# Performance work log

Hardware: AMD Instinct MI355X
Metric: run time of the kernel (lower is better)

Reference implementation:

```python
import jax, jax.numpy as jnp
import numpy as np

WS = 7        # window_size
NH = 3        # num_heads


def setup_inputs() -> dict:
    key = jax.random.key(0)
    ks = jax.random.split(key, 5)
    B, H, W, C = 8, 224, 224, 96
    s = 1.0 / np.sqrt(C)
    x = jax.random.normal(ks[0], (B, H, W, C), dtype=jnp.float32)
    qkv_w = jax.random.normal(ks[1], (C, 3 * C), dtype=jnp.float32) * s
    qkv_b = jnp.zeros((3 * C,), dtype=jnp.float32)
    proj_w = jax.random.normal(ks[2], (C, C), dtype=jnp.float32) * s
    proj_b = jnp.zeros((C,), dtype=jnp.float32)
    return {"x": x, "qkv_w": qkv_w, "qkv_b": qkv_b, "proj_w": proj_w, "proj_b": proj_b}


def reference(x, qkv_w, qkv_b, proj_w, proj_b):
    B, H, W, C = x.shape
    ws, nh = WS, NH
    hd = C // nh
    pad_h = (ws - H % ws) % ws
    pad_w = (ws - W % ws) % ws
    x = jnp.pad(x, ((0, 0), (0, pad_h), (0, pad_w), (0, 0)))
    Hp, Wp = x.shape[1], x.shape[2]
    # window partition: [B,Hp,Wp,C] -> [B*nWh*nWw, ws*ws, C]
    xw = x.reshape(B, Hp // ws, ws, Wp // ws, ws, C)
    xw = xw.transpose(0, 1, 3, 2, 4, 5).reshape(-1, ws * ws, C)
    nW = xw.shape[0]
    qkv = xw @ qkv_w + qkv_b                      # [nW, ws*ws, 3C]
    q, k, v = jnp.split(qkv, 3, axis=-1)
    def heads(t):
        return t.reshape(nW, ws * ws, nh, hd).transpose(0, 2, 1, 3)  # [nW,nh,L,hd]
    q, k, v = heads(q), heads(k), heads(v)
    scale = 1.0 / np.sqrt(hd).astype(np.float32)
    attn = jnp.einsum('whld,whmd->whlm', q, k) * scale
    attn = jax.nn.softmax(attn, axis=-1)
    o = jnp.einsum('whlm,whmd->whld', attn, v)    # [nW,nh,L,hd]
    o = o.transpose(0, 2, 1, 3).reshape(nW, ws * ws, C)
    o = o @ proj_w + proj_b
    # window merge: inverse of partition
    o = o.reshape(B, Hp // ws, Wp // ws, ws, ws, C)
    o = o.transpose(0, 1, 3, 2, 4, 5).reshape(B, Hp, Wp, C)
    return o[:, :H, :W, :]
```

## Files before the change

kernel.cpp:

```cpp
#include <hip/hip_runtime.h>
#include <stdint.h>

typedef __bf16 bf16;
typedef __bf16 bf16x4 __attribute__((ext_vector_type(4)));
typedef __bf16 bf16x8 __attribute__((ext_vector_type(8)));
typedef float  f32x4  __attribute__((ext_vector_type(4)));

#define MFMA16(a,b,c) __builtin_amdgcn_mfma_f32_16x16x32_bf16((a),(b),(c),0,0,0)

#define XS_STR 104
#define QK_STR 200
#define SB_STR 72
#define S_HEAD 4608

__global__ void prep_weights(const float* __restrict__ qkv_w,
                             const float* __restrict__ proj_w,
                             bf16* __restrict__ wT) {
    int i = blockIdx.x * 256 + threadIdx.x;
    if (i < 288 * 96) {
        int j = i / 96, c = i - j * 96;
        wT[i] = (bf16)qkv_w[c * 288 + j];
    } else if (i < 288 * 96 + 96 * 96) {
        int t = i - 288 * 96;
        int j = t / 96, c = t - j * 96;
        wT[i] = (bf16)proj_w[c * 96 + j];
    }
}

__global__ __launch_bounds__(256, 4)
void win_attn_kernel(const float* __restrict__ x,
                     const float* __restrict__ qkv_b,
                     const float* __restrict__ proj_b,
                     const bf16* __restrict__ qkvwT,
                     const bf16* __restrict__ projwT,
                     float* __restrict__ out)
{
    __shared__ bf16 ldsA[64 * XS_STR];
    __shared__ bf16 ldsB[3 * 64 * SB_STR];

    const int tid  = threadIdx.x;
    const int wid  = tid >> 6;
    const int lane = tid & 63;
    const int lm   = lane & 15;
    const int lq   = lane >> 4;

    const int wi = blockIdx.x;
    const int b  = wi >> 10;
    const int wr = wi & 1023;
    const int h0 = (wr >> 5) * 7;
    const int w0 = (wr & 31) * 7;

    {
        const float* xbase = x + ((size_t)(b * 224 + h0) * 224 + w0) * 96;
        #pragma unroll
        for (int kk = 0; kk < 3; ++kk) {
            const int t   = tid + kk * 256;
            const int pix = t / 12;
            const int f8  = t - pix * 12;
            bf16x8 bv = {};
            if (pix < 49) {
                const int pr = pix / 7, pc = pix - pr * 7;
                const float* p = xbase + ((size_t)pr * 224 + pc) * 96 + f8 * 8;
                const float4 v0 = *(const float4*)p;
                const float4 v1 = *(const float4*)(p + 4);
                bv = (bf16x8){ (bf16)v0.x, (bf16)v0.y, (bf16)v0.z, (bf16)v0.w,
                               (bf16)v1.x, (bf16)v1.y, (bf16)v1.z, (bf16)v1.w };
            }
            *(bf16x8*)&ldsA[pix * XS_STR + f8 * 8] = bv;
        }
    }
    __syncthreads();

    bf16x8 afr[4][3];
    #pragma unroll
    for (int tt = 0; tt < 4; ++tt)
        #pragma unroll
        for (int ks = 0; ks < 3; ++ks)
            afr[tt][ks] = *(const bf16x8*)&ldsA[(tt * 16 + lm) * XS_STR + ks * 32 + lq * 8];
    __syncthreads();

    {
        const float Cs = 0.2550348607051632f;
        for (int ft = wid; ft < 18; ft += 4) {
            bf16x8 wf[3];
            #pragma unroll
            for (int ks = 0; ks < 3; ++ks)
                wf[ks] = *(const bf16x8*)&qkvwT[(size_t)(ft * 16 + lm) * 96 + ks * 32 + lq * 8];
            if (ft < 12) {
                const f32x4 bias4 = *(const f32x4*)(qkv_b + ft * 16 + lq * 4);
                f32x4 acc[4];
                #pragma unroll
                for (int tt = 0; tt < 4; ++tt) acc[tt] = bias4;
                #pragma unroll
                for (int ks = 0; ks < 3; ++ks)
                    #pragma unroll
                    for (int tt = 0; tt < 4; ++tt)
                        acc[tt] = MFMA16(wf[ks], afr[tt][ks], acc[tt]);
                const bool isq = (ft < 6);
                #pragma unroll
                for (int tt = 0; tt < 4; ++tt) {
                    f32x4 a = acc[tt];
                    if (isq) a *= Cs;
                    bf16x4 pv = { (bf16)a[0], (bf16)a[1], (bf16)a[2], (bf16)a[3] };
                    *(bf16x4*)&ldsB[(tt * 16 + lm) * QK_STR + ft * 16 + lq * 4] = pv;
                }
            } else {
                const int d0 = (ft - 12) * 16 + lm;
                const float bias = qkv_b[192 + d0];
                f32x4 acc[4];
                #pragma unroll
                for (int mt = 0; mt < 4; ++mt) acc[mt] = (f32x4){bias, bias, bias, bias};
                #pragma unroll
                for (int ks = 0; ks < 3; ++ks)
                    #pragma unroll
                    for (int mt = 0; mt < 4; ++mt)
                        acc[mt] = MFMA16(afr[mt][ks], wf[ks], acc[mt]);
                #pragma unroll
                for (int mt = 0; mt < 4; ++mt) {
                    bf16x4 pv = { (bf16)acc[mt][0], (bf16)acc[mt][1],
                                  (bf16)acc[mt][2], (bf16)acc[mt][3] };
                    const int grp = mt * 2 + (lq >> 1);
                    *(bf16x4*)&ldsA[d0 * 64 + ((grp ^ (d0 & 7)) << 3) + ((lq & 1) << 2)] = pv;
                }
            }
        }
    }
    __syncthreads();

    bf16x8 aq[4], bk[4];
    if (wid < 3) {
        const int h = wid;
        #pragma unroll
        for (int qt = 0; qt < 4; ++qt)
            aq[qt] = *(const bf16x8*)&ldsB[(qt * 16 + lm) * QK_STR + h * 32 + lq * 8];
        #pragma unroll
        for (int kt = 0; kt < 4; ++kt)
            bk[kt] = *(const bf16x8*)&ldsB[(kt * 16 + lm) * QK_STR + 96 + h * 32 + lq * 8];
    }
    __syncthreads();

    f32x4 oacc[2][4];
    f32x4 rin;
    if (wid < 3) {
        const int h = wid;
        const f32x4 zf = {0.f, 0.f, 0.f, 0.f};
        bf16* Sb = &ldsB[h * S_HEAD];
        f32x4 sums = zf;

        #pragma unroll
        for (int kt = 0; kt < 4; ++kt) {
            f32x4 s[4];
            #pragma unroll
            for (int qt = 0; qt < 4; ++qt)
                s[qt] = MFMA16(bk[kt], aq[qt], zf);
            if (kt < 3) {
                #pragma unroll
                for (int qt = 0; qt < 4; ++qt) {
                    const float p0 = exp2f(s[qt][0]);
                    const float p1 = exp2f(s[qt][1]);
                    const float p2 = exp2f(s[qt][2]);
                    const float p3 = exp2f(s[qt][3]);
                    sums[qt] += (p0 + p1) + (p2 + p3);
                    bf16x4 pv = { (bf16)p0, (bf16)p1, (bf16)p2, (bf16)p3 };
                    *(bf16x4*)&Sb[(qt * 16 + lm) * SB_STR + kt * 16 + lq * 4] = pv;
                }
            } else {
                #pragma unroll
                for (int qt = 0; qt < 4; ++qt) {
                    const float p0 = (lq == 0) ? exp2f(s[qt][0]) : 0.f;
                    sums[qt] += p0;
                    bf16x4 pv = { (bf16)p0, (bf16)0.f, (bf16)0.f, (bf16)0.f };
                    *(bf16x4*)&Sb[(qt * 16 + lm) * SB_STR + 48 + lq * 4] = pv;
                }
            }
        }
        #pragma unroll
        for (int qt = 0; qt < 4; ++qt) {
            float sm = sums[qt];
            sm += __shfl_xor(sm, 16);
            sm += __shfl_xor(sm, 32);
            rin[qt] = __builtin_amdgcn_rcpf(sm);
        }
        asm volatile("s_waitcnt lgkmcnt(0)" ::: "memory");

        #pragma unroll
        for (int f2 = 0; f2 < 2; ++f2)
            #pragma unroll
            for (int qt = 0; qt < 4; ++qt) oacc[f2][qt] = zf;
        #pragma unroll
        for (int ks = 0; ks < 2; ++ks) {
            bf16x8 av[2], ap[4];
            #pragma unroll
            for (int f2 = 0; f2 < 2; ++f2) {
                const int frow = h * 32 + f2 * 16 + lm;
                av[f2] = *(const bf16x8*)&ldsA[frow * 64 + (((ks * 4 + lq) ^ (frow & 7)) << 3)];
            }
            #pragma unroll
            for (int qt = 0; qt < 4; ++qt)
                ap[qt] = *(const bf16x8*)&Sb[(qt * 16 + lm) * SB_STR + ks * 32 + lq * 8];
            #pragma unroll
            for (int f2 = 0; f2 < 2; ++f2)
                #pragma unroll
                for (int qt = 0; qt < 4; ++qt)
                    oacc[f2][qt] = MFMA16(av[f2], ap[qt], oacc[f2][qt]);
        }
        #pragma unroll
        for (int f2 = 0; f2 < 2; ++f2)
            #pragma unroll
            for (int qt = 0; qt < 4; ++qt)
                oacc[f2][qt] *= rin[qt];
    }
    __syncthreads();

    if (wid < 3) {
        const int h = wid;
        #pragma unroll
        for (int f2 = 0; f2 < 2; ++f2)
            #pragma unroll
            for (int qt = 0; qt < 4; ++qt) {
                const f32x4 a = oacc[f2][qt];
                bf16x4 ov = { (bf16)a[0], (bf16)a[1], (bf16)a[2], (bf16)a[3] };
                *(bf16x4*)&ldsB[(qt * 16 + lm) * XS_STR + h * 32 + f2 * 16 + lq * 4] = ov;
            }
    }
    __syncthreads();

    {
        const int tt = wid;
        bf16x8 of[3];
        #pragma unroll
        for (int ks = 0; ks < 3; ++ks)
            of[ks] = *(const bf16x8*)&ldsB[(tt * 16 + lm) * XS_STR + ks * 32 + lq * 8];
        const int token = tt * 16 + lm;
        const int tv = (token < 49) ? token : 0;
        const int pr = tv / 7, pc = tv - pr * 7;
        float* obase = out + ((size_t)(b * 224 + h0 + pr) * 224 + (w0 + pc)) * 96 + lq * 4;
        #pragma unroll
        for (int ft = 0; ft < 6; ++ft) {
            bf16x8 wp[3];
            #pragma unroll
            for (int ks = 0; ks < 3; ++ks)
                wp[ks] = *(const bf16x8*)&projwT[(size_t)(ft * 16 + lm) * 96 + ks * 32 + lq * 8];
            f32x4 acc = *(const f32x4*)(proj_b + ft * 16 + lq * 4);
            #pragma unroll
            for (int ks = 0; ks < 3; ++ks)
                acc = MFMA16(wp[ks], of[ks], acc);
            if (token < 49)
                *(f32x4*)(obase + ft * 16) = acc;
        }
    }
}

extern "C" void kernel_launch(void* const* d_in, const int* in_sizes, int n_in,
                              void* d_out, int out_size, void* d_ws, size_t ws_size,
                              hipStream_t stream) {
    const float* x      = (const float*)d_in[0];
    const float* qkv_w  = (const float*)d_in[1];
    const float* qkv_b  = (const float*)d_in[2];
    const float* proj_w = (const float*)d_in[3];
    const float* proj_b = (const float*)d_in[4];
    float* out = (float*)d_out;

    bf16* wT = (bf16*)d_ws;
    const int n_w = 288 * 96 + 96 * 96;
    prep_weights<<<(n_w + 255) / 256, 256, 0, stream>>>(qkv_w, proj_w, wT);
    win_attn_kernel<<<8192, 256, 0, stream>>>(x, qkv_b, proj_b,
                                              wT, wT + 288 * 96, out);
}
```

Before: 334.5 us.

## Split attention by query tiles across all four waves and shrink LDS footprint

Reassigns the attention stage so each of the four waves handles one 16-row query tile across all three heads, instead of three waves each handling one head over all query tiles. Softmax probabilities now stay in registers and are fed straight into the PV MFMA, which removes the score round-trip through LDS and two barriers. LDS is consolidated into one 49-row-padded buffer (~32KB) and launch bounds rise to 5 blocks per CU to raise occupancy. The cost is some repeated K/V fragment loads per wave, more register pressure under the tighter bound, and garbage padding rows handled by masking.

```diff
diff --git a/kernel.cpp b/kernel.cpp
--- a/kernel.cpp
+++ b/kernel.cpp
@@ -8,10 +8,11 @@
 
 #define MFMA16(a,b,c) __builtin_amdgcn_mfma_f32_16x16x32_bf16((a),(b),(c),0,0,0)
 
-#define XS_STR 104
-#define QK_STR 200
-#define SB_STR 72
-#define S_HEAD 4608
+#define ST 104
+#define QB 0
+#define KB 5096
+#define VB 10192
+#define LDS_ELEMS 16336
 
 __global__ void prep_weights(const float* __restrict__ qkv_w,
                              const float* __restrict__ proj_w,
@@ -27,7 +28,7 @@
     }
 }
 
-__global__ __launch_bounds__(256, 4)
+__global__ __launch_bounds__(256, 5)
 void win_attn_kernel(const float* __restrict__ x,
                      const float* __restrict__ qkv_b,
                      const float* __restrict__ proj_b,
@@ -35,8 +36,7 @@
                      const bf16* __restrict__ projwT,
                      float* __restrict__ out)
 {
-    __shared__ bf16 ldsA[64 * XS_STR];
-    __shared__ bf16 ldsB[3 * 64 * SB_STR];
+    __shared__ bf16 lds[LDS_ELEMS];
 
     const int tid  = threadIdx.x;
     const int wid  = tid >> 6;
@@ -52,21 +52,15 @@
 
     {
         const float* xbase = x + ((size_t)(b * 224 + h0) * 224 + w0) * 96;
-        #pragma unroll
-        for (int kk = 0; kk < 3; ++kk) {
-            const int t   = tid + kk * 256;
-            const int pix = t / 12;
-            const int f8  = t - pix * 12;
-            bf16x8 bv = {};
-            if (pix < 49) {
-                const int pr = pix / 7, pc = pix - pr * 7;
-                const float* p = xbase + ((size_t)pr * 224 + pc) * 96 + f8 * 8;
-                const float4 v0 = *(const float4*)p;
-                const float4 v1 = *(const float4*)(p + 4);
-                bv = (bf16x8){ (bf16)v0.x, (bf16)v0.y, (bf16)v0.z, (bf16)v0.w,
-                               (bf16)v1.x, (bf16)v1.y, (bf16)v1.z, (bf16)v1.w };
-            }
-            *(bf16x8*)&ldsA[pix * XS_STR + f8 * 8] = bv;
+        for (int t = tid; t < 49 * 12; t += 256) {
+            const int pix = t / 12, f8 = t - pix * 12;
+            const int pr = pix / 7, pc = pix - pr * 7;
+            const float* p = xbase + ((size_t)pr * 224 + pc) * 96 + f8 * 8;
+            const float4 v0 = *(const float4*)p;
+            const float4 v1 = *(const float4*)(p + 4);
+            bf16x8 bv = { (bf16)v0.x, (bf16)v0.y, (bf16)v0.z, (bf16)v0.w,
+                          (bf16)v1.x, (bf16)v1.y, (bf16)v1.z, (bf16)v1.w };
+            *(bf16x8*)&lds[VB + pix * ST + f8 * 8] = bv;
         }
     }
     __syncthreads();
@@ -75,8 +69,12 @@
     #pragma unroll
     for (int tt = 0; tt < 4; ++tt)
         #pragma unroll
-        for (int ks = 0; ks < 3; ++ks)
-            afr[tt][ks] = *(const bf16x8*)&ldsA[(tt * 16 + lm) * XS_STR + ks * 32 + lq * 8];
+        for (int ks = 0; ks < 3; ++ks) {
+            if (tt < 3 || lm == 0)
+                afr[tt][ks] = *(const bf16x8*)&lds[VB + (tt * 16 + lm) * ST + ks * 32 + lq * 8];
+            else
+                afr[tt][ks] = (bf16x8){};
+        }
     __syncthreads();
 
     {
@@ -97,12 +95,16 @@
                     for (int tt = 0; tt < 4; ++tt)
                         acc[tt] = MFMA16(wf[ks], afr[tt][ks], acc[tt]);
                 const bool isq = (ft < 6);
+                const int base = isq ? QB : KB;
+                const int col  = (isq ? ft : ft - 6) * 16 + lq * 4;
                 #pragma unroll
                 for (int tt = 0; tt < 4; ++tt) {
-                    f32x4 a = acc[tt];
-                    if (isq) a *= Cs;
-                    bf16x4 pv = { (bf16)a[0], (bf16)a[1], (bf16)a[2], (bf16)a[3] };
-                    *(bf16x4*)&ldsB[(tt * 16 + lm) * QK_STR + ft * 16 + lq * 4] = pv;
+                    if (tt < 3 || lm == 0) {
+                        f32x4 a = acc[tt];
+                        if (isq) a *= Cs;
+                        bf16x4 pv = { (bf16)a[0], (bf16)a[1], (bf16)a[2], (bf16)a[3] };
+                        *(bf16x4*)&lds[base + (tt * 16 + lm) * ST + col] = pv;
+                    }
                 }
             } else {
                 const int d0 = (ft - 12) * 16 + lm;
@@ -119,109 +121,62 @@
                 for (int mt = 0; mt < 4; ++mt) {
                     bf16x4 pv = { (bf16)acc[mt][0], (bf16)acc[mt][1],
                                   (bf16)acc[mt][2], (bf16)acc[mt][3] };
-                    const int grp = mt * 2 + (lq >> 1);
-                    *(bf16x4*)&ldsA[d0 * 64 + ((grp ^ (d0 & 7)) << 3) + ((lq & 1) << 2)] = pv;
+                    const int g = (mt >> 1) * 4 + lq;
+                    *(bf16x4*)&lds[VB + d0 * 64 + ((g ^ (d0 & 7)) << 3) + ((mt & 1) << 2)] = pv;
                 }
             }
         }
     }
     __syncthreads();
 
-    bf16x8 aq[4], bk[4];
-    if (wid < 3) {
-        const int h = wid;
-        #pragma unroll
-        for (int qt = 0; qt < 4; ++qt)
-            aq[qt] = *(const bf16x8*)&ldsB[(qt * 16 + lm) * QK_STR + h * 32 + lq * 8];
-        #pragma unroll
-        for (int kt = 0; kt < 4; ++kt)
-            bk[kt] = *(const bf16x8*)&ldsB[(kt * 16 + lm) * QK_STR + 96 + h * 32 + lq * 8];
-    }
-    __syncthreads();
-
-    f32x4 oacc[2][4];
-    f32x4 rin;
-    if (wid < 3) {
-        const int h = wid;
+    {
+        const int qrow = wid * 16 + lm;
         const f32x4 zf = {0.f, 0.f, 0.f, 0.f};
-        bf16* Sb = &ldsB[h * S_HEAD];
-        f32x4 sums = zf;
-
-        #pragma unroll
-        for (int kt = 0; kt < 4; ++kt) {
-            f32x4 s[4];
-            #pragma unroll
-            for (int qt = 0; qt < 4; ++qt)
-                s[qt] = MFMA16(bk[kt], aq[qt], zf);
-            if (kt < 3) {
-                #pragma unroll
-                for (int qt = 0; qt < 4; ++qt) {
-                    const float p0 = exp2f(s[qt][0]);
-                    const float p1 = exp2f(s[qt][1]);
-                    const float p2 = exp2f(s[qt][2]);
-                    const float p3 = exp2f(s[qt][3]);
-                    sums[qt] += (p0 + p1) + (p2 + p3);
-                    bf16x4 pv = { (bf16)p0, (bf16)p1, (bf16)p2, (bf16)p3 };
-                    *(bf16x4*)&Sb[(qt * 16 + lm) * SB_STR + kt * 16 + lq * 4] = pv;
-                }
-            } else {
-                #pragma unroll
-                for (int qt = 0; qt < 4; ++qt) {
-                    const float p0 = (lq == 0) ? exp2f(s[qt][0]) : 0.f;
-                    sums[qt] += p0;
-                    bf16x4 pv = { (bf16)p0, (bf16)0.f, (bf16)0.f, (bf16)0.f };
-                    *(bf16x4*)&Sb[(qt * 16 + lm) * SB_STR + 48 + lq * 4] = pv;
-                }
+        #pragma unroll
+        for (int h = 0; h < 3; ++h) {
+            const bf16x8 aqv = *(const bf16x8*)&lds[QB + qrow * ST + h * 32 + lq * 8];
+            bf16x8 bkv[4];
+            #pragma unroll
+            for (int kt = 0; kt < 4; ++kt)
+                bkv[kt] = *(const bf16x8*)&lds[KB + (kt * 16 + lm) * ST + h * 32 + lq * 8];
+            f32x4 s0 = MFMA16(bkv[0], aqv, zf);
+            f32x4 s1 = MFMA16(bkv[1], aqv, zf);
+            f32x4 s2 = MFMA16(bkv[2], aqv, zf);
+            f32x4 s3 = MFMA16(bkv[3], aqv, zf);
+            float p0  = exp2f(s0[0]), p1  = exp2f(s0[1]), p2  = exp2f(s0[2]), p3  = exp2f(s0[3]);
+            float p4  = exp2f(s1[0]), p5  = exp2f(s1[1]), p6  = exp2f(s1[2]), p7  = exp2f(s1[3]);
+            float p8  = exp2f(s2[0]), p9  = exp2f(s2[1]), p10 = exp2f(s2[2]), p11 = exp2f(s2[3]);
+            float p48 = (lq == 0) ? exp2f(s3[0]) : 0.f;
+            float part = ((p0 + p1) + (p2 + p3)) + ((p4 + p5) + (p6 + p7))
+                       + ((p8 + p9) + (p10 + p11)) + p48;
+            part += __shfl_xor(part, 16);
+            part += __shfl_xor(part, 32);
+            const float rin = __builtin_amdgcn_rcpf(part);
+            bf16x8 ap0 = { (bf16)p0, (bf16)p1, (bf16)p2,  (bf16)p3,
+                           (bf16)p4, (bf16)p5, (bf16)p6,  (bf16)p7 };
+            bf16x8 ap1 = { (bf16)p8, (bf16)p9, (bf16)p10, (bf16)p11,
+                           (bf16)p48, (bf16)0.f, (bf16)0.f, (bf16)0.f };
+            bf16x8 av00, av01, av10, av11;
+            {
+                const int fr0 = h * 32 + lm, fr1 = h * 32 + 16 + lm;
+                av00 = *(const bf16x8*)&lds[VB + fr0 * 64 + (((0 + lq) ^ (fr0 & 7)) << 3)];
+                av01 = *(const bf16x8*)&lds[VB + fr1 * 64 + (((0 + lq) ^ (fr1 & 7)) << 3)];
+                av10 = *(const bf16x8*)&lds[VB + fr0 * 64 + (((4 + lq) ^ (fr0 & 7)) << 3)];
+                av11 = *(const bf16x8*)&lds[VB + fr1 * 64 + (((4 + lq) ^ (fr1 & 7)) << 3)];
             }
-        }
-        #pragma unroll
-        for (int qt = 0; qt < 4; ++qt) {
-            float sm = sums[qt];
-            sm += __shfl_xor(sm, 16);
-            sm += __shfl_xor(sm, 32);
-            rin[qt] = __builtin_amdgcn_rcpf(sm);
-        }
-        asm volatile("s_waitcnt lgkmcnt(0)" ::: "memory");
-
-        #pragma unroll
-        for (int f2 = 0; f2 < 2; ++f2)
-            #pragma unroll
-            for (int qt = 0; qt < 4; ++qt) oacc[f2][qt] = zf;
-        #pragma unroll
-        for (int ks = 0; ks < 2; ++ks) {
-            bf16x8 av[2], ap[4];
-            #pragma unroll
-            for (int f2 = 0; f2 < 2; ++f2) {
-                const int frow = h * 32 + f2 * 16 + lm;
-                av[f2] = *(const bf16x8*)&ldsA[frow * 64 + (((ks * 4 + lq) ^ (frow & 7)) << 3)];
+            f32x4 o0 = MFMA16(av00, ap0, zf);
+            o0 = MFMA16(av10, ap1, o0);
+            f32x4 o1 = MFMA16(av01, ap0, zf);
+            o1 = MFMA16(av11, ap1, o1);
+            o0 *= rin;
+            o1 *= rin;
+            if (wid < 3 || lm == 0) {
+                bf16x4 w0v = { (bf16)o0[0], (bf16)o0[1], (bf16)o0[2], (bf16)o0[3] };
+                bf16x4 w1v = { (bf16)o1[0], (bf16)o1[1], (bf16)o1[2], (bf16)o1[3] };
+                *(bf16x4*)&lds[QB + qrow * ST + h * 32 + lq * 4]      = w0v;
+                *(bf16x4*)&lds[QB + qrow * ST + h * 32 + 16 + lq * 4] = w1v;
             }
-            #pragma unroll
-            for (int qt = 0; qt < 4; ++qt)
-                ap[qt] = *(const bf16x8*)&Sb[(qt * 16 + lm) * SB_STR + ks * 32 + lq * 8];
-            #pragma unroll
-            for (int f2 = 0; f2 < 2; ++f2)
-                #pragma unroll
-                for (int qt = 0; qt < 4; ++qt)
-                    oacc[f2][qt] = MFMA16(av[f2], ap[qt], oacc[f2][qt]);
-        }
-        #pragma unroll
-        for (int f2 = 0; f2 < 2; ++f2)
-            #pragma unroll
-            for (int qt = 0; qt < 4; ++qt)
-                oacc[f2][qt] *= rin[qt];
-    }
-    __syncthreads();
-
-    if (wid < 3) {
-        const int h = wid;
-        #pragma unroll
-        for (int f2 = 0; f2 < 2; ++f2)
-            #pragma unroll
-            for (int qt = 0; qt < 4; ++qt) {
-                const f32x4 a = oacc[f2][qt];
-                bf16x4 ov = { (bf16)a[0], (bf16)a[1], (bf16)a[2], (bf16)a[3] };
-                *(bf16x4*)&ldsB[(qt * 16 + lm) * XS_STR + h * 32 + f2 * 16 + lq * 4] = ov;
-            }
+        }
     }
     __syncthreads();
 
@@ -230,7 +185,7 @@
         bf16x8 of[3];
         #pragma unroll
         for (int ks = 0; ks < 3; ++ks)
-            of[ks] = *(const bf16x8*)&ldsB[(tt * 16 + lm) * XS_STR + ks * 32 + lq * 8];
+            of[ks] = *(const bf16x8*)&lds[QB + (tt * 16 + lm) * ST + ks * 32 + lq * 8];
         const int token = tt * 16 + lm;
         const int tv = (token < 49) ? token : 0;
         const int pr = tv / 7, pc = tv - pr * 7;
```

New measurement: 341.5 us. +2.1%, slower.
